# Kernel optimization log

Hardware: AMD Instinct MI355X
Metric: run time of the kernel (lower is better)

Reference implementation:

```python
import jax, jax.numpy as jnp
import numpy as np

B, N, D = 32, 264, 375          # subjects, nets per subject, net feature dim
P = N * (N - 1) // 2            # 34716 pairs -> ClassificationNet input
RRELU_SLOPE = 11.0 / 48.0       # eval-mode RReLU: (lower+upper)/2 = (1/8+1/3)/2


def _rrelu(x):
    return jnp.where(x >= 0, x, x * RRELU_SLOPE)


def setup_inputs() -> dict:
    key = jax.random.key(0)
    ks = jax.random.split(key, 23)
    w = lambda k, s: (jax.random.normal(k, s, jnp.float32) * 0.02)
    b = lambda k, n: (jax.random.normal(k, (n,), jnp.float32) * 0.01)
    return {
        "x": jax.random.normal(ks[0], (B, N, D), jnp.float32),
        # FeatureExtractor(375, 32)
        "fe_w1": w(ks[1], (D, 64)),  "fe_b1": b(ks[2], 64),
        "fe_w2": w(ks[3], (64, 64)), "fe_b2": b(ks[4], 64),
        "fe_w3": w(ks[5], (64, 32)), "fe_b3": b(ks[6], 32),
        # SimilarityMeasureNetwork
        "sm_w1": w(ks[7], (64, 32)),  "sm_b1": b(ks[8], 32),
        "sm_w2": w(ks[9], (32, 16)),  "sm_b2": b(ks[10], 16),
        "sm_w3": w(ks[11], (16, 8)),  "sm_b3": b(ks[12], 8),
        "sm_w4": w(ks[13], (8, 1)),   "sm_b4": b(ks[14], 1),
        # ClassificationNet(34716, 3)
        "cl_w1": w(ks[15], (P, 4096)),   "cl_b1": b(ks[16], 4096),
        "cl_w2": w(ks[17], (4096, 256)), "cl_b2": b(ks[18], 256),
        "cl_w3": w(ks[19], (256, 64)),   "cl_b3": b(ks[20], 64),
        "cl_w4": w(ks[21], (64, 3)),     "cl_b4": b(ks[22], 3),
    }


def reference(x, fe_w1, fe_b1, fe_w2, fe_b2, fe_w3, fe_b3,
              sm_w1, sm_b1, sm_w2, sm_b2, sm_w3, sm_b3, sm_w4, sm_b4,
              cl_w1, cl_b1, cl_w2, cl_b2, cl_w3, cl_b3, cl_w4, cl_b4):
    # Feature extractor over all (subject, net) at once: [B, N, 375] -> [B, N, 32]
    h = _rrelu(x @ fe_w1 + fe_b1)            # dropout is identity in eval
    h = jax.nn.relu(h @ fe_w2 + fe_b2)
    feats = h @ fe_w3 + fe_b3                # [B, N, 32]

    # All unordered net pairs (i < j), matching the nested python loop order
    i1, i2 = np.triu_indices(N, k=1)
    pair = jnp.concatenate([feats[:, i1], feats[:, i2]], axis=-1)  # [B, P, 64]

    # Similarity MLP -> one tanh scalar per pair
    s = jax.nn.relu(pair @ sm_w1 + sm_b1)
    s = jax.nn.relu(s @ sm_w2 + sm_b2)
    s = jax.nn.relu(s @ sm_w3 + sm_b3)
    s = jnp.tanh(s @ sm_w4 + sm_b4)[..., 0]  # [B, P]

    # Classification head with log_softmax
    c = _rrelu(s @ cl_w1 + cl_b1)            # dropout identity in eval
    c = jax.nn.relu(c @ cl_w2 + cl_b2)
    c = jax.nn.relu(c @ cl_w3 + cl_b3)
    c = c @ cl_w4 + cl_b4                    # [B, 3]
    return jax.nn.log_softmax(c, axis=-1)
```

## Files before the change

### kernel.cpp

```cpp
#include <hip/hip_runtime.h>
#include <hip/hip_bf16.h>

#define RRELU_SLOPE (11.0f / 48.0f)

#define NB 32
#define NN 264
#define ND 375
#define NP 34716

__global__ __launch_bounds__(256) void fe_uv_kernel(
    const float* __restrict__ x,
    const float* __restrict__ w1, const float* __restrict__ b1,
    const float* __restrict__ w2, const float* __restrict__ b2,
    const float* __restrict__ w3, const float* __restrict__ b3,
    const float* __restrict__ smw1, const float* __restrict__ smb1,
    float* __restrict__ U, float* __restrict__ V)
{
    __shared__ float h[4][64];
    const int lane = threadIdx.x & 63;
    const int wave = threadIdx.x >> 6;
    const int row  = blockIdx.x * 4 + wave;
    const int urow = __builtin_amdgcn_readfirstlane(row);
    const float* xr = x + (size_t)urow * ND;

    float a1 = b1[lane];
#pragma unroll 5
    for (int d = 0; d < ND; ++d)
        a1 = fmaf(xr[d], w1[d * 64 + lane], a1);
    a1 = (a1 >= 0.f) ? a1 : a1 * RRELU_SLOPE;
    h[wave][lane] = a1;
    __syncthreads();

    float a2 = b2[lane];
#pragma unroll 8
    for (int c = 0; c < 64; ++c)
        a2 = fmaf(h[wave][c], w2[c * 64 + lane], a2);
    a2 = fmaxf(a2, 0.f);
    __syncthreads();
    h[wave][lane] = a2;
    __syncthreads();

    const int o = lane & 31;
    float f = b3[o];
#pragma unroll 8
    for (int c = 0; c < 64; ++c)
        f = fmaf(h[wave][c], w3[c * 32 + o], f);
    __syncthreads();
    if (lane < 32) h[wave][lane] = f;
    __syncthreads();

    const float* sw = smw1 + ((lane < 32) ? 0 : 32 * 32);
    float uv = (lane < 32) ? smb1[o] : 0.f;
#pragma unroll 8
    for (int c = 0; c < 32; ++c)
        uv = fmaf(h[wave][c], sw[c * 32 + o], uv);

    const int bb = urow / NN;
    const int nn = urow - bb * NN;
    float* dst = ((lane < 32) ? U : V) + ((size_t)nn * 32 + bb) * 32 + o;
    *dst = uv;
}

__device__ __forceinline__ int cfun(int i) {
    return i * NN - (i * (i + 1)) / 2;
}

__global__ __launch_bounds__(256) void sim_kernel(
    const float* __restrict__ U, const float* __restrict__ V,
    const float* __restrict__ w2, const float* __restrict__ b2,
    const float* __restrict__ w3, const float* __restrict__ b3,
    const float* __restrict__ w4, const float* __restrict__ b4,
    float* __restrict__ sT)
{
    const int t = threadIdx.x;
    const int b = t & 31;
    const int p = blockIdx.x * 8 + (t >> 5);
    if (p >= NP) return;

    int i = (int)((527.0f - sqrtf(277729.0f - 8.0f * (float)p)) * 0.5f);
    i = max(0, min(NN - 2, i));
    while (i < NN - 2 && cfun(i + 1) <= p) ++i;
    while (i > 0 && cfun(i) > p) --i;
    const int j = i + 1 + (p - cfun(i));

    const float4* u4 = (const float4*)(U + ((size_t)i * 32 + b) * 32);
    const float4* v4 = (const float4*)(V + ((size_t)j * 32 + b) * 32);
    float h1[32];
#pragma unroll
    for (int q = 0; q < 8; ++q) {
        float4 uu = u4[q], vv = v4[q];
        h1[q * 4 + 0] = fmaxf(uu.x + vv.x, 0.f);
        h1[q * 4 + 1] = fmaxf(uu.y + vv.y, 0.f);
        h1[q * 4 + 2] = fmaxf(uu.z + vv.z, 0.f);
        h1[q * 4 + 3] = fmaxf(uu.w + vv.w, 0.f);
    }

    float h2[16];
#pragma unroll
    for (int o = 0; o < 16; ++o) h2[o] = b2[o];
#pragma unroll
    for (int c = 0; c < 32; ++c)
#pragma unroll
        for (int o = 0; o < 16; ++o)
            h2[o] = fmaf(h1[c], w2[c * 16 + o], h2[o]);
#pragma unroll
    for (int o = 0; o < 16; ++o) h2[o] = fmaxf(h2[o], 0.f);

    float h3[8];
#pragma unroll
    for (int o = 0; o < 8; ++o) h3[o] = b3[o];
#pragma unroll
    for (int c = 0; c < 16; ++c)
#pragma unroll
        for (int o = 0; o < 8; ++o)
            h3[o] = fmaf(h2[c], w3[c * 8 + o], h3[o]);
#pragma unroll
    for (int o = 0; o < 8; ++o) h3[o] = fmaxf(h3[o], 0.f);

    float z = b4[0];
#pragma unroll
    for (int c = 0; c < 8; ++c) z = fmaf(h3[c], w4[c], z);

    sT[(size_t)p * 32 + b] = tanhf(z);
}

__global__ __launch_bounds__(256) void gemm_splitk(
    const float* __restrict__ aT, const float* __restrict__ w,
    float* __restrict__ partial, int K, int N, int chunk)
{
    const int n  = blockIdx.x * 256 + threadIdx.x;
    const int ns = blockIdx.y;
    const int k0 = ns * chunk;
    const int k1 = min(k0 + chunk, K);

    float acc[32];
#pragma unroll
    for (int m = 0; m < 32; ++m) acc[m] = 0.f;

    const float* wp = w + (size_t)k0 * N + n;
#pragma unroll 4
    for (int k = k0; k < k1; ++k) {
        const float wv = *wp; wp += N;
        const float4* a4 = (const float4*)(aT + (size_t)k * 32);
#pragma unroll
        for (int mq = 0; mq < 8; ++mq) {
            float4 av = a4[mq];
            acc[mq * 4 + 0] = fmaf(av.x, wv, acc[mq * 4 + 0]);
            acc[mq * 4 + 1] = fmaf(av.y, wv, acc[mq * 4 + 1]);
            acc[mq * 4 + 2] = fmaf(av.z, wv, acc[mq * 4 + 2]);
            acc[mq * 4 + 3] = fmaf(av.w, wv, acc[mq * 4 + 3]);
        }
    }

    float* po = partial + ((size_t)ns * N + n) * 32;
#pragma unroll
    for (int m = 0; m < 32; ++m) po[m] = acc[m];
}

__global__ __launch_bounds__(256) void reduce_act(
    const float* __restrict__ partial, const float* __restrict__ bias,
    float* __restrict__ out, int NT, int ns_count, int mode)
{
    const int idx = blockIdx.x * 256 + threadIdx.x;
    const int n = idx >> 5;
    float s = bias[n];
#pragma unroll 4
    for (int ns = 0; ns < ns_count; ++ns)
        s += partial[(size_t)ns * NT + idx];
    out[idx] = (mode == 0) ? ((s >= 0.f) ? s : s * RRELU_SLOPE) : fmaxf(s, 0.f);
}

__global__ __launch_bounds__(256) void layer3_kernel(
    const float* __restrict__ c2T, const float* __restrict__ w3,
    const float* __restrict__ b3, float* __restrict__ c3T)
{
    const int t = threadIdx.x;
    const int b = t & 31;
    const int o = blockIdx.x * 8 + (t >> 5);
    float acc = b3[o];
#pragma unroll 8
    for (int k = 0; k < 256; ++k)
        acc = fmaf(c2T[k * 32 + b], w3[k * 64 + o], acc);
    c3T[o * 32 + b] = fmaxf(acc, 0.f);
}

__global__ __launch_bounds__(128) void final_kernel(
    const float* __restrict__ c3T, const float* __restrict__ w4,
    const float* __restrict__ b4, float* __restrict__ out)
{
    __shared__ float c4s[96];
    __shared__ float lse[32];
    const int t = threadIdx.x;
    if (t < 96) {
        const int b = t / 3, j = t - b * 3;
        float acc = b4[j];
#pragma unroll
        for (int c = 0; c < 64; ++c)
            acc = fmaf(c3T[c * 32 + b], w4[c * 3 + j], acc);
        c4s[t] = acc;
    }
    __syncthreads();
    if (t < 32) {
        const float a0 = c4s[t * 3], a1 = c4s[t * 3 + 1], a2 = c4s[t * 3 + 2];
        const float m = fmaxf(a0, fmaxf(a1, a2));
        lse[t] = m + logf(expf(a0 - m) + expf(a1 - m) + expf(a2 - m));
    }
    __syncthreads();
    if (t < 96) out[t] = c4s[t] - lse[t / 3];
}

extern "C" void kernel_launch(void* const* d_in, const int* in_sizes, int n_in,
                              void* d_out, int out_size, void* d_ws, size_t ws_size,
                              hipStream_t stream)
{
    const float* x     = (const float*)d_in[0];
    const float* fe_w1 = (const float*)d_in[1];
    const float* fe_b1 = (const float*)d_in[2];
    const float* fe_w2 = (const float*)d_in[3];
    const float* fe_b2 = (const float*)d_in[4];
    const float* fe_w3 = (const float*)d_in[5];
    const float* fe_b3 = (const float*)d_in[6];
    const float* sm_w1 = (const float*)d_in[7];
    const float* sm_b1 = (const float*)d_in[8];
    const float* sm_w2 = (const float*)d_in[9];
    const float* sm_b2 = (const float*)d_in[10];
    const float* sm_w3 = (const float*)d_in[11];
    const float* sm_b3 = (const float*)d_in[12];
    const float* sm_w4 = (const float*)d_in[13];
    const float* sm_b4 = (const float*)d_in[14];
    const float* cl_w1 = (const float*)d_in[15];
    const float* cl_b1 = (const float*)d_in[16];
    const float* cl_w2 = (const float*)d_in[17];
    const float* cl_b2 = (const float*)d_in[18];
    const float* cl_w3 = (const float*)d_in[19];
    const float* cl_b3 = (const float*)d_in[20];
    const float* cl_w4 = (const float*)d_in[21];
    const float* cl_b4 = (const float*)d_in[22];

    float* ws  = (float*)d_ws;
    float* U   = ws;
    float* V   = U   + 270336;
    float* sT  = V   + 270336;
    float* p1  = sT  + 1110912;
    float* c1T = p1  + 4194304;
    float* p2  = c1T + 131072;
    float* c2T = p2  + 1048576;
    float* c3T = c2T + 8192;

    hipLaunchKernelGGL(fe_uv_kernel, dim3(2112), dim3(256), 0, stream,
                       x, fe_w1, fe_b1, fe_w2, fe_b2, fe_w3, fe_b3,
                       sm_w1, sm_b1, U, V);
    hipLaunchKernelGGL(sim_kernel, dim3((NP + 7) / 8), dim3(256), 0, stream,
                       U, V, sm_w2, sm_b2, sm_w3, sm_b3, sm_w4, sm_b4, sT);
    hipLaunchKernelGGL(gemm_splitk, dim3(16, 32), dim3(256), 0, stream,
                       sT, cl_w1, p1, NP, 4096, 1085);
    hipLaunchKernelGGL(reduce_act, dim3(512), dim3(256), 0, stream,
                       p1, cl_b1, c1T, 4096 * 32, 32, 0);
    hipLaunchKernelGGL(gemm_splitk, dim3(1, 128), dim3(256), 0, stream,
                       c1T, cl_w2, p2, 4096, 256, 32);
    hipLaunchKernelGGL(reduce_act, dim3(32), dim3(256), 0, stream,
                       p2, cl_b2, c2T, 256 * 32, 128, 1);
    hipLaunchKernelGGL(layer3_kernel, dim3(8), dim3(256), 0, stream,
                       c2T, cl_w3, cl_b3, c3T);
    hipLaunchKernelGGL(final_kernel, dim3(1), dim3(128), 0, stream,
                       c3T, cl_w4, cl_b4, (float*)d_out);
}
```

Before: 1.069 ms.

## Interleave U/V layout for coalesced sim loads and stage GEMM activations in LDS

U and V are now stored as [net][channel-quad][batch][4], so the 32 batch lanes of sim_kernel read consecutive float4s and the loads coalesce. The layer-2 accumulation is folded into the load loop, which shortens the live range of h1. gemm_splitk now copies 256-row tiles of the activation matrix into shared memory and reads them from LDS instead of global memory, with unroll 8. Both kernels get launch_bounds(256,1). That hint can allow more registers per thread but may reduce occupancy, and the 32KB LDS tile also limits how many blocks fit per CU.

After: 1.297 ms. 1.21x slower.

```diff
diff --git a/kernel.cpp b/kernel.cpp
--- a/kernel.cpp
+++ b/kernel.cpp
@@ -57,7 +57,8 @@
 
     const int bb = urow / NN;
     const int nn = urow - bb * NN;
-    float* dst = ((lane < 32) ? U : V) + ((size_t)nn * 32 + bb) * 32 + o;
+    float* dst = ((lane < 32) ? U : V)
+               + (((size_t)nn * 8 + (o >> 2)) * 32 + bb) * 4 + (o & 3);
     *dst = uv;
 }
 
@@ -65,7 +66,7 @@
     return i * NN - (i * (i + 1)) / 2;
 }
 
-__global__ __launch_bounds__(256) void sim_kernel(
+__global__ __launch_bounds__(256, 1) void sim_kernel(
     const float* __restrict__ U, const float* __restrict__ V,
     const float* __restrict__ w2, const float* __restrict__ b2,
     const float* __restrict__ w3, const float* __restrict__ b3,
@@ -83,26 +84,27 @@
     while (i > 0 && cfun(i) > p) --i;
     const int j = i + 1 + (p - cfun(i));
 
-    const float4* u4 = (const float4*)(U + ((size_t)i * 32 + b) * 32);
-    const float4* v4 = (const float4*)(V + ((size_t)j * 32 + b) * 32);
-    float h1[32];
+    const float4* u4 = (const float4*)U + (size_t)i * 256 + b;
+    const float4* v4 = (const float4*)V + (size_t)j * 256 + b;
+
+    float h2[16];
+#pragma unroll
+    for (int o = 0; o < 16; ++o) h2[o] = b2[o];
+
 #pragma unroll
     for (int q = 0; q < 8; ++q) {
-        float4 uu = u4[q], vv = v4[q];
-        h1[q * 4 + 0] = fmaxf(uu.x + vv.x, 0.f);
-        h1[q * 4 + 1] = fmaxf(uu.y + vv.y, 0.f);
-        h1[q * 4 + 2] = fmaxf(uu.z + vv.z, 0.f);
-        h1[q * 4 + 3] = fmaxf(uu.w + vv.w, 0.f);
-    }
-
-    float h2[16];
-#pragma unroll
-    for (int o = 0; o < 16; ++o) h2[o] = b2[o];
-#pragma unroll
-    for (int c = 0; c < 32; ++c)
-#pragma unroll
-        for (int o = 0; o < 16; ++o)
-            h2[o] = fmaf(h1[c], w2[c * 16 + o], h2[o]);
+        float4 uu = u4[q * 32], vv = v4[q * 32];
+        float h1c[4];
+        h1c[0] = fmaxf(uu.x + vv.x, 0.f);
+        h1c[1] = fmaxf(uu.y + vv.y, 0.f);
+        h1c[2] = fmaxf(uu.z + vv.z, 0.f);
+        h1c[3] = fmaxf(uu.w + vv.w, 0.f);
+#pragma unroll
+        for (int c = 0; c < 4; ++c)
+#pragma unroll
+            for (int o = 0; o < 16; ++o)
+                h2[o] = fmaf(h1c[c], w2[(q * 4 + c) * 16 + o], h2[o]);
+    }
 #pragma unroll
     for (int o = 0; o < 16; ++o) h2[o] = fmaxf(h2[o], 0.f);
 
@@ -124,10 +126,11 @@
     sT[(size_t)p * 32 + b] = tanhf(z);
 }
 
-__global__ __launch_bounds__(256) void gemm_splitk(
+__global__ __launch_bounds__(256, 1) void gemm_splitk(
     const float* __restrict__ aT, const float* __restrict__ w,
     float* __restrict__ partial, int K, int N, int chunk)
 {
+    __shared__ float sa[256 * 32];
     const int n  = blockIdx.x * 256 + threadIdx.x;
     const int ns = blockIdx.y;
     const int k0 = ns * chunk;
@@ -138,17 +141,27 @@
     for (int m = 0; m < 32; ++m) acc[m] = 0.f;
 
     const float* wp = w + (size_t)k0 * N + n;
-#pragma unroll 4
-    for (int k = k0; k < k1; ++k) {
-        const float wv = *wp; wp += N;
-        const float4* a4 = (const float4*)(aT + (size_t)k * 32);
-#pragma unroll
-        for (int mq = 0; mq < 8; ++mq) {
-            float4 av = a4[mq];
-            acc[mq * 4 + 0] = fmaf(av.x, wv, acc[mq * 4 + 0]);
-            acc[mq * 4 + 1] = fmaf(av.y, wv, acc[mq * 4 + 1]);
-            acc[mq * 4 + 2] = fmaf(av.z, wv, acc[mq * 4 + 2]);
-            acc[mq * 4 + 3] = fmaf(av.w, wv, acc[mq * 4 + 3]);
+    for (int kt = k0; kt < k1; kt += 256) {
+        const int klen = min(256, k1 - kt);
+        __syncthreads();
+        const float4* src  = (const float4*)(aT + (size_t)kt * 32);
+        float4*       dstl = (float4*)sa;
+        for (int idx = threadIdx.x; idx < klen * 8; idx += 256)
+            dstl[idx] = src[idx];
+        __syncthreads();
+
+#pragma unroll 8
+        for (int k = 0; k < klen; ++k) {
+            const float wv = *wp; wp += N;
+            const float4* a4 = (const float4*)(sa + k * 32);
+#pragma unroll
+            for (int mq = 0; mq < 8; ++mq) {
+                float4 av = a4[mq];
+                acc[mq * 4 + 0] = fmaf(av.x, wv, acc[mq * 4 + 0]);
+                acc[mq * 4 + 1] = fmaf(av.y, wv, acc[mq * 4 + 1]);
+                acc[mq * 4 + 2] = fmaf(av.z, wv, acc[mq * 4 + 2]);
+                acc[mq * 4 + 3] = fmaf(av.w, wv, acc[mq * 4 + 3]);
+            }
         }
     }
 
```
